# Optimization experiments

Measured on AMD Instinct MI355X. Metric: run time of the kernel, lower is better.

## Reference

```python
import jax, jax.numpy as jnp
import numpy as np

N_NODES = 100000
N_EDGES = 1600000
IN_CH, HID_CH, OUT_CH = 128, 128, 64


def glorot(key, fan_in, fan_out):
    lim = np.sqrt(6.0 / (fan_in + fan_out)).astype(np.float32)
    return jax.random.uniform(key, (fan_in, fan_out), jnp.float32, -lim, lim)


def gcn_conv(x, src, dst, W, b):
    """PyG GCNConv: add self-loops, symmetric deg^-1/2 normalization,
    linear transform, scatter-add aggregation at targets, plus bias."""
    n = x.shape[0]
    xw = x @ W  # [N, F_out]
    loop = jnp.arange(n)
    s = jnp.concatenate([src, loop])  # sources (message origin)
    d = jnp.concatenate([dst, loop])  # targets (aggregation site)
    deg = jax.ops.segment_sum(jnp.ones_like(d, dtype=xw.dtype), d, num_segments=n)
    dinv = jnp.where(deg > 0, jax.lax.rsqrt(deg), 0.0)
    norm = dinv[s] * dinv[d]  # [E+N]
    out = jax.ops.segment_sum(norm[:, None] * xw[s], d, num_segments=n)
    return out + b


def setup_inputs() -> dict:
    key = jax.random.key(0)
    ks = jax.random.split(key, 8)
    x = jax.random.normal(ks[0], (N_NODES, IN_CH), jnp.float32)
    edge_index = jax.random.randint(ks[1], (2, N_EDGES), 0, N_NODES, jnp.int64)
    return {
        "x": x,
        "edge_index": edge_index,
        "W1": glorot(ks[2], IN_CH, HID_CH),
        "b1": jnp.zeros((HID_CH,), jnp.float32),
        "W2": glorot(ks[3], HID_CH, HID_CH),
        "b2": jnp.zeros((HID_CH,), jnp.float32),
        "W3": glorot(ks[4], HID_CH, OUT_CH),
        "b3": jnp.zeros((OUT_CH,), jnp.float32),
    }


def reference(x, edge_index, W1, b1, W2, b2, W3, b3):
    src, dst = edge_index[0], edge_index[1]
    # eval mode: dropout is identity
    h = jax.nn.relu(gcn_conv(x, src, dst, W1, b1))
    h = jax.nn.relu(gcn_conv(h, src, dst, W2, b2))
    h = gcn_conv(h, src, dst, W3, b3)
    return jax.nn.log_softmax(h, axis=1)
```

## Files before the change

kernel.cpp:

```cpp
#include <hip/hip_runtime.h>
#include <math.h>


#define NN 100000
#define NE 1600000
#define NBUK 391
#define BCAP 4608

typedef float floatx4 __attribute__((ext_vector_type(4)));
typedef short short8 __attribute__((ext_vector_type(8)));

__device__ __forceinline__ unsigned short f2bf(float f) {
    unsigned u = __float_as_uint(f);
    unsigned r = (u + 0x7fffu + ((u >> 16) & 1u)) >> 16;
    return (unsigned short)r;
}
__device__ __forceinline__ float bflo(unsigned u) { return __uint_as_float(u << 16); }
__device__ __forceinline__ float bfhi(unsigned u) { return __uint_as_float(u & 0xffff0000u); }

__global__ __launch_bounds__(256) void k_wprep_all(const float* __restrict__ W1, const float* __restrict__ W2,
                                                   const float* __restrict__ W3,
                                                   unsigned short* __restrict__ wt1, unsigned short* __restrict__ wt2,
                                                   unsigned short* __restrict__ wt3, int* __restrict__ bcur) {
    if (blockIdx.x == 0) {
        bcur[threadIdx.x] = 0;
        bcur[threadIdx.x + 256] = 0;
    }
    int idx = blockIdx.x * 256 + threadIdx.x;
    if (idx < 16384) {
        int n = idx >> 7, k = idx & 127;
        wt1[idx] = f2bf(W1[k * 128 + n]);
    } else if (idx < 32768) {
        int i = idx - 16384;
        int n = i >> 7, k = i & 127;
        wt2[i] = f2bf(W2[k * 128 + n]);
    } else if (idx < 40960) {
        int i = idx - 32768;
        int n = i >> 7, k = i & 127;
        wt3[i] = f2bf(W3[k * 64 + n]);
    }
}

__global__ __launch_bounds__(256) void k_bucket(const int4* __restrict__ src4, const int4* __restrict__ dst4,
                                                int* __restrict__ bcur, int* __restrict__ bbuf, int E) {
    __shared__ int hist[NBUK];
    __shared__ int base[NBUK];
    int t = threadIdx.x;
    for (int b = t; b < NBUK; b += 256) hist[b] = 0;
    __syncthreads();
    int E4 = E >> 2;
    int q0 = blockIdx.x * 1024;
    int4 sv[4], dv[4];
    bool valid[4];
    #pragma unroll
    for (int j = 0; j < 4; j++) {
        int q = q0 + j * 256 + t;
        valid[j] = (q < E4);
        if (valid[j]) {
            sv[j] = src4[q];
            dv[j] = dst4[q];
            atomicAdd(&hist[dv[j].x >> 8], 1);
            atomicAdd(&hist[dv[j].y >> 8], 1);
            atomicAdd(&hist[dv[j].z >> 8], 1);
            atomicAdd(&hist[dv[j].w >> 8], 1);
        }
    }
    __syncthreads();
    for (int b = t; b < NBUK; b += 256) {
        int c = hist[b];
        base[b] = c ? atomicAdd(&bcur[b], c) : 0;
        hist[b] = 0;
    }
    __syncthreads();
    #pragma unroll
    for (int j = 0; j < 4; j++) {
        if (valid[j]) {
            int ss[4] = {sv[j].x, sv[j].y, sv[j].z, sv[j].w};
            int dd[4] = {dv[j].x, dv[j].y, dv[j].z, dv[j].w};
            #pragma unroll
            for (int u = 0; u < 4; u++) {
                int b = dd[u] >> 8;
                int r = atomicAdd(&hist[b], 1);
                int pos = base[b] + r;
                if (pos < BCAP) bbuf[b * BCAP + pos] = (ss[u] << 8) | (dd[u] & 255);
            }
        }
    }
}

__global__ __launch_bounds__(256) void k_build(const int* __restrict__ bcur, const int* __restrict__ bbuf,
                                               int* __restrict__ row_ptr, int* __restrict__ csr,
                                               float* __restrict__ dinv, int N, int E) {
    __shared__ int sh[256];
    __shared__ int cur[256];
    __shared__ int red[256];
    __shared__ int loc[BCAP];
    int b = blockIdx.x, t = threadIdx.x;
    int cnt = min(bcur[b], BCAP);
    int partial = 0;
    for (int j = t; j < b; j += 256) partial += min(bcur[j], BCAP);
    red[t] = partial;
    sh[t] = 0;
    __syncthreads();
    #pragma unroll
    for (int o = 128; o > 0; o >>= 1) {
        if (t < o) red[t] += red[t + o];
        __syncthreads();
    }
    int gbase = red[0];
    const int* bp = bbuf + b * BCAP;
    for (int i = t; i < cnt; i += 256) atomicAdd(&sh[bp[i] & 255], 1);
    __syncthreads();
    int v = sh[t];
    for (int o = 1; o < 256; o <<= 1) {
        int u = (t >= o) ? sh[t - o] : 0;
        __syncthreads();
        sh[t] += u;
        __syncthreads();
    }
    int excl = sh[t] - v;
    int node = b * 256 + t;
    if (node < N) {
        row_ptr[node] = gbase + excl;
        dinv[node] = rsqrtf((float)v + 1.0f);
    }
    if (b == NBUK - 1 && t == 0) row_ptr[N] = gbase + cnt;
    cur[t] = excl;
    __syncthreads();
    for (int i = t; i < cnt; i += 256) {
        int p = bp[i];
        int r = atomicAdd(&cur[p & 255], 1);
        loc[r] = p >> 8;
    }
    __syncthreads();
    for (int i = t; i < cnt; i += 256) csr[gbase + i] = loc[i];
}


template <int NC, bool CVT>
__global__ __launch_bounds__(256) void k_mfma(const void* __restrict__ Av, const unsigned short* __restrict__ Wtg,
                                              const float* __restrict__ dinv, unsigned short* __restrict__ Y, int M) {
    constexpr int K = 128;
    constexpr int NT = NC / 16;
    constexpr int NU = NC / 32;
    __shared__ unsigned short Wt[NC][136];
    __shared__ unsigned short Ost[4][16][NC + 8];
    int t = threadIdx.x;
    for (int idx = t; idx < NC * 16; idx += 256) {
        int nrow = idx >> 4, chunk = idx & 15;
        *(uint4*)&Wt[nrow][chunk * 8] = *(const uint4*)(Wtg + nrow * K + chunk * 8);
    }
    __syncthreads();
    int lane = t & 63, wid = t >> 6;
    int col = lane & 15, quad = lane >> 4;
    int nstrips = M / 16;
    int stride = gridDim.x * 4;
    int s = blockIdx.x * 4 + wid;
    if (s >= nstrips) return;

    auto loadA = [&](int strip, short8 af[4]) {
        int row0 = strip * 16;
        if (CVT) {
            const float* Af = (const float*)Av + (size_t)(row0 + col) * K + quad * 8;
            #pragma unroll
            for (int ks = 0; ks < 4; ks++) {
                float4 f0 = *(const float4*)(Af + ks * 32);
                float4 f1 = *(const float4*)(Af + ks * 32 + 4);
                short8 v;
                v[0] = (short)f2bf(f0.x); v[1] = (short)f2bf(f0.y); v[2] = (short)f2bf(f0.z); v[3] = (short)f2bf(f0.w);
                v[4] = (short)f2bf(f1.x); v[5] = (short)f2bf(f1.y); v[6] = (short)f2bf(f1.z); v[7] = (short)f2bf(f1.w);
                af[ks] = v;
            }
        } else {
            const unsigned short* Ab = (const unsigned short*)Av + (size_t)(row0 + col) * K + quad * 8;
            #pragma unroll
            for (int ks = 0; ks < 4; ks++) af[ks] = *(const short8*)(Ab + ks * 32);
        }
    };

    short8 cur[4];
    loadA(s, cur);
    while (true) {
        int snext = s + stride;
        bool has = (snext < nstrips);
        short8 nxt[4];
        if (has) loadA(snext, nxt);

        floatx4 acc[NT];
        #pragma unroll
        for (int i = 0; i < NT; i++) acc[i] = (floatx4){0.f, 0.f, 0.f, 0.f};
        #pragma unroll
        for (int ks = 0; ks < 4; ks++) {
            #pragma unroll
            for (int nt = 0; nt < NT; nt++) {
                short8 bfrag = *(const short8*)&Wt[nt * 16 + col][ks * 32 + quad * 8];
                acc[nt] = __builtin_amdgcn_mfma_f32_16x16x32_bf16(cur[ks], bfrag, acc[nt], 0, 0, 0);
            }
        }
        int row0 = s * 16;
        #pragma unroll
        for (int r = 0; r < 4; r++) {
            float dv = dinv[row0 + quad * 4 + r];
            #pragma unroll
            for (int nt = 0; nt < NT; nt++)
                Ost[wid][quad * 4 + r][nt * 16 + col] = f2bf(acc[nt][r] * dv);
        }
        #pragma unroll
        for (int i = 0; i < NU; i++) {
            int idx = i * 64 + lane;
            int rr = (NC == 128) ? (idx >> 4) : (idx >> 3);
            int cc = (NC == 128) ? (idx & 15) : (idx & 7);
            ((uint4*)&Y[(size_t)(row0 + rr) * NC])[cc] = *(uint4*)&Ost[wid][rr][cc * 8];
        }
        if (!has) break;
        s = snext;
        #pragma unroll
        for (int ks = 0; ks < 4; ks++) cur[ks] = nxt[ks];
    }
}


__device__ __forceinline__ void acc8(float* a, uint4 v) {
    a[0] += bflo(v.x); a[1] += bfhi(v.x);
    a[2] += bflo(v.y); a[3] += bfhi(v.y);
    a[4] += bflo(v.z); a[5] += bfhi(v.z);
    a[6] += bflo(v.w); a[7] += bfhi(v.w);
}

__global__ __launch_bounds__(256) void k_gather_relu_bf(const uint4* __restrict__ y, const int* __restrict__ csr,
                                                        const int* __restrict__ row_ptr, const float* __restrict__ dinv,
                                                        const float* __restrict__ bias, uint4* __restrict__ h, int n) {
    int half = blockIdx.x & 1;
    int node = (blockIdx.x >> 1) * 32 + (threadIdx.x >> 3);
    int c = (threadIdx.x & 7) + half * 8;
    if (node >= n) return;
    int s0 = row_ptr[node], s1 = row_ptr[node + 1];
    float a[8] = {};
    acc8(a, y[(size_t)node * 16 + c]);
    int p = s0;
    for (; p + 4 <= s1; p += 4) {
        int i0 = csr[p], i1 = csr[p + 1], i2 = csr[p + 2], i3 = csr[p + 3];
        uint4 v0 = y[(size_t)i0 * 16 + c];
        uint4 v1 = y[(size_t)i1 * 16 + c];
        uint4 v2 = y[(size_t)i2 * 16 + c];
        uint4 v3 = y[(size_t)i3 * 16 + c];
        acc8(a, v0); acc8(a, v1); acc8(a, v2); acc8(a, v3);
    }
    for (; p < s1; p++) acc8(a, y[(size_t)csr[p] * 16 + c]);
    float s = dinv[node];
    float4 b0 = ((const float4*)bias)[c * 2];
    float4 b1 = ((const float4*)bias)[c * 2 + 1];
    float r0 = fmaxf(s * a[0] + b0.x, 0.f), r1 = fmaxf(s * a[1] + b0.y, 0.f);
    float r2 = fmaxf(s * a[2] + b0.z, 0.f), r3 = fmaxf(s * a[3] + b0.w, 0.f);
    float r4 = fmaxf(s * a[4] + b1.x, 0.f), r5 = fmaxf(s * a[5] + b1.y, 0.f);
    float r6 = fmaxf(s * a[6] + b1.z, 0.f), r7 = fmaxf(s * a[7] + b1.w, 0.f);
    uint4 o;
    o.x = ((unsigned)f2bf(r1) << 16) | f2bf(r0);
    o.y = ((unsigned)f2bf(r3) << 16) | f2bf(r2);
    o.z = ((unsigned)f2bf(r5) << 16) | f2bf(r4);
    o.w = ((unsigned)f2bf(r7) << 16) | f2bf(r6);
    h[(size_t)node * 16 + c] = o;
}

__global__ __launch_bounds__(256) void k_gather_lsm_bf(const uint4* __restrict__ y, const int* __restrict__ csr,
                                                       const int* __restrict__ row_ptr, const float* __restrict__ dinv,
                                                       const float* __restrict__ bias, float4* __restrict__ out4, int n) {
    int node = blockIdx.x * 32 + (threadIdx.x >> 3);
    int c = threadIdx.x & 7;
    if (node >= n) return;
    int s0 = row_ptr[node], s1 = row_ptr[node + 1];
    float a[8] = {};
    acc8(a, y[(size_t)node * 8 + c]);
    int p = s0;
    for (; p + 4 <= s1; p += 4) {
        int i0 = csr[p], i1 = csr[p + 1], i2 = csr[p + 2], i3 = csr[p + 3];
        uint4 v0 = y[(size_t)i0 * 8 + c];
        uint4 v1 = y[(size_t)i1 * 8 + c];
        uint4 v2 = y[(size_t)i2 * 8 + c];
        uint4 v3 = y[(size_t)i3 * 8 + c];
        acc8(a, v0); acc8(a, v1); acc8(a, v2); acc8(a, v3);
    }
    for (; p < s1; p++) acc8(a, y[(size_t)csr[p] * 8 + c]);
    float s = dinv[node];
    float4 b0 = ((const float4*)bias)[c * 2];
    float4 b1 = ((const float4*)bias)[c * 2 + 1];
    float v[8];
    v[0] = s * a[0] + b0.x; v[1] = s * a[1] + b0.y; v[2] = s * a[2] + b0.z; v[3] = s * a[3] + b0.w;
    v[4] = s * a[4] + b1.x; v[5] = s * a[5] + b1.y; v[6] = s * a[6] + b1.z; v[7] = s * a[7] + b1.w;
    float m = v[0];
    #pragma unroll
    for (int i = 1; i < 8; i++) m = fmaxf(m, v[i]);
    #pragma unroll
    for (int o = 4; o > 0; o >>= 1) m = fmaxf(m, __shfl_xor(m, o));
    float sum = 0.f;
    #pragma unroll
    for (int i = 0; i < 8; i++) sum += expf(v[i] - m);
    #pragma unroll
    for (int o = 4; o > 0; o >>= 1) sum += __shfl_xor(sum, o);
    float lse = m + logf(sum);
    out4[(size_t)node * 16 + c * 2]     = make_float4(v[0] - lse, v[1] - lse, v[2] - lse, v[3] - lse);
    out4[(size_t)node * 16 + c * 2 + 1] = make_float4(v[4] - lse, v[5] - lse, v[6] - lse, v[7] - lse);
}


extern "C" void kernel_launch(void* const* d_in, const int* in_sizes, int n_in,
                              void* d_out, int out_size, void* d_ws, size_t ws_size,
                              hipStream_t stream) {
    const float* x  = (const float*)d_in[0];
    const int*   ei = (const int*)d_in[1];
    const float* W1 = (const float*)d_in[2];
    const float* b1 = (const float*)d_in[3];
    const float* W2 = (const float*)d_in[4];
    const float* b2 = (const float*)d_in[5];
    const float* W3 = (const float*)d_in[6];
    const float* b3 = (const float*)d_in[7];
    float* out = (float*)d_out;

    const int N = NN, E = NE;

    char* ws = (char*)d_ws;
    size_t off = 0;
    auto alloc = [&](size_t bytes) -> void* {
        void* p = ws + off;
        off += bytes;
        off = (off + 255) & ~(size_t)255;
        return p;
    };
    int*            row_ptr = (int*)alloc((size_t)(N + 1) * 4);
    float*          dinvv   = (float*)alloc((size_t)N * 4);
    int*            bcur    = (int*)alloc(512 * 4);
    int*            bbuf    = (int*)alloc((size_t)NBUK * BCAP * 4);
    int*            csr     = (int*)alloc((size_t)E * 4);
    unsigned short* wt1     = (unsigned short*)alloc(128 * 128 * 2);
    unsigned short* wt2     = (unsigned short*)alloc(128 * 128 * 2);
    unsigned short* wt3     = (unsigned short*)alloc(64 * 128 * 2);
    unsigned short* yb      = (unsigned short*)alloc((size_t)N * 128 * 2);
    unsigned short* hb      = (unsigned short*)alloc((size_t)N * 128 * 2);
    (void)ws_size; (void)in_sizes; (void)n_in; (void)out_size;

    const int* srcp = ei;
    const int* dstp = ei + E;

    k_wprep_all<<<160, 256, 0, stream>>>(W1, W2, W3, wt1, wt2, wt3, bcur);
    k_bucket<<<(E + 4095) / 4096, 256, 0, stream>>>((const int4*)srcp, (const int4*)dstp, bcur, bbuf, E);
    k_build<<<NBUK, 256, 0, stream>>>(bcur, bbuf, row_ptr, csr, dinvv, N, E);

    k_mfma<128, true><<<768, 256, 0, stream>>>(x, wt1, dinvv, yb, N);
    k_gather_relu_bf<<<(N / 32) * 2, 256, 0, stream>>>((const uint4*)yb, csr, row_ptr, dinvv, b1, (uint4*)hb, N);
    k_mfma<128, false><<<768, 256, 0, stream>>>(hb, wt2, dinvv, yb, N);
    k_gather_relu_bf<<<(N / 32) * 2, 256, 0, stream>>>((const uint4*)yb, csr, row_ptr, dinvv, b2, (uint4*)hb, N);
    k_mfma<64, false><<<768, 256, 0, stream>>>(hb, wt3, dinvv, yb, N);
    k_gather_lsm_bf<<<N / 32, 256, 0, stream>>>((const uint4*)yb, csr, row_ptr, dinvv, b3, (float4*)out, N);
}
```

Before: 319.6 us.

## Fuse edge bucketing, first-layer GEMM and weight prep into one front kernel

```diff
diff --git a/kernel.cpp b/kernel.cpp
--- a/kernel.cpp
+++ b/kernel.cpp
@@ -6,6 +6,7 @@
 #define NE 1600000
 #define NBUK 391
 #define BCAP 4608
+#define MFMA_BLKS 768
 
 typedef float floatx4 __attribute__((ext_vector_type(4)));
 typedef short short8 __attribute__((ext_vector_type(8)));
@@ -18,72 +19,144 @@
 __device__ __forceinline__ float bflo(unsigned u) { return __uint_as_float(u << 16); }
 __device__ __forceinline__ float bfhi(unsigned u) { return __uint_as_float(u & 0xffff0000u); }
 
-__global__ __launch_bounds__(256) void k_wprep_all(const float* __restrict__ W1, const float* __restrict__ W2,
-                                                   const float* __restrict__ W3,
-                                                   unsigned short* __restrict__ wt1, unsigned short* __restrict__ wt2,
-                                                   unsigned short* __restrict__ wt3, int* __restrict__ bcur) {
-    if (blockIdx.x == 0) {
-        bcur[threadIdx.x] = 0;
-        bcur[threadIdx.x + 256] = 0;
-    }
-    int idx = blockIdx.x * 256 + threadIdx.x;
-    if (idx < 16384) {
-        int n = idx >> 7, k = idx & 127;
-        wt1[idx] = f2bf(W1[k * 128 + n]);
-    } else if (idx < 32768) {
-        int i = idx - 16384;
-        int n = i >> 7, k = i & 127;
-        wt2[i] = f2bf(W2[k * 128 + n]);
-    } else if (idx < 40960) {
-        int i = idx - 32768;
-        int n = i >> 7, k = i & 127;
-        wt3[i] = f2bf(W3[k * 64 + n]);
-    }
-}
-
-__global__ __launch_bounds__(256) void k_bucket(const int4* __restrict__ src4, const int4* __restrict__ dst4,
-                                                int* __restrict__ bcur, int* __restrict__ bbuf, int E) {
-    __shared__ int hist[NBUK];
-    __shared__ int base[NBUK];
+__global__ __launch_bounds__(256) void k_front(const int4* __restrict__ src4, const int4* __restrict__ dst4,
+                                               int* __restrict__ bcur, int* __restrict__ bbuf, int E,
+                                               const float* __restrict__ x, const float* __restrict__ W1,
+                                               unsigned short* __restrict__ Y, int M,
+                                               const float* __restrict__ W2, const float* __restrict__ W3,
+                                               unsigned short* __restrict__ wt2, unsigned short* __restrict__ wt3) {
+    __shared__ union {
+        struct { int hist[NBUK]; int base[NBUK]; } bk;
+        struct { unsigned short Wt[128][136]; unsigned short Ost[4][16][136]; } mm;
+    } u;
     int t = threadIdx.x;
-    for (int b = t; b < NBUK; b += 256) hist[b] = 0;
-    __syncthreads();
-    int E4 = E >> 2;
-    int q0 = blockIdx.x * 1024;
-    int4 sv[4], dv[4];
-    bool valid[4];
-    #pragma unroll
-    for (int j = 0; j < 4; j++) {
-        int q = q0 + j * 256 + t;
-        valid[j] = (q < E4);
-        if (valid[j]) {
-            sv[j] = src4[q];
-            dv[j] = dst4[q];
-            atomicAdd(&hist[dv[j].x >> 8], 1);
-            atomicAdd(&hist[dv[j].y >> 8], 1);
-            atomicAdd(&hist[dv[j].z >> 8], 1);
-            atomicAdd(&hist[dv[j].w >> 8], 1);
-        }
-    }
-    __syncthreads();
-    for (int b = t; b < NBUK; b += 256) {
-        int c = hist[b];
-        base[b] = c ? atomicAdd(&bcur[b], c) : 0;
-        hist[b] = 0;
-    }
-    __syncthreads();
-    #pragma unroll
-    for (int j = 0; j < 4; j++) {
-        if (valid[j]) {
-            int ss[4] = {sv[j].x, sv[j].y, sv[j].z, sv[j].w};
-            int dd[4] = {dv[j].x, dv[j].y, dv[j].z, dv[j].w};
-            #pragma unroll
-            for (int u = 0; u < 4; u++) {
-                int b = dd[u] >> 8;
-                int r = atomicAdd(&hist[b], 1);
-                int pos = base[b] + r;
-                if (pos < BCAP) bbuf[b * BCAP + pos] = (ss[u] << 8) | (dd[u] & 255);
-            }
+    int blk = blockIdx.x;
+
+    if (blk < NBUK) {
+        for (int b = t; b < NBUK; b += 256) u.bk.hist[b] = 0;
+        __syncthreads();
+        int E4 = E >> 2;
+        int q0 = blk * 1024;
+        int4 sv[4], dv[4];
+        bool valid[4];
+        #pragma unroll
+        for (int j = 0; j < 4; j++) {
+            int q = q0 + j * 256 + t;
+            valid[j] = (q < E4);
+            if (valid[j]) {
+                sv[j] = src4[q];
+                dv[j] = dst4[q];
+                atomicAdd(&u.bk.hist[dv[j].x >> 8], 1);
+                atomicAdd(&u.bk.hist[dv[j].y >> 8], 1);
+                atomicAdd(&u.bk.hist[dv[j].z >> 8], 1);
+                atomicAdd(&u.bk.hist[dv[j].w >> 8], 1);
+            }
+        }
+        __syncthreads();
+        for (int b = t; b < NBUK; b += 256) {
+            int c = u.bk.hist[b];
+            u.bk.base[b] = c ? atomicAdd(&bcur[b], c) : 0;
+            u.bk.hist[b] = 0;
+        }
+        __syncthreads();
+        #pragma unroll
+        for (int j = 0; j < 4; j++) {
+            if (valid[j]) {
+                int ss[4] = {sv[j].x, sv[j].y, sv[j].z, sv[j].w};
+                int dd[4] = {dv[j].x, dv[j].y, dv[j].z, dv[j].w};
+                #pragma unroll
+                for (int w = 0; w < 4; w++) {
+                    int b = dd[w] >> 8;
+                    int r = atomicAdd(&u.bk.hist[b], 1);
+                    int pos = u.bk.base[b] + r;
+                    if (pos < BCAP) bbuf[b * BCAP + pos] = (ss[w] << 8) | (dd[w] & 255);
+                }
+            }
+        }
+        return;
+    }
+
+    if (blk >= NBUK + MFMA_BLKS) {
+        int idx = (blk - NBUK - MFMA_BLKS) * 256 + t;
+        if (idx < 16384) {
+            int n = idx >> 7, k = idx & 127;
+            wt2[idx] = f2bf(W2[k * 128 + n]);
+        } else if (idx < 24576) {
+            int i = idx - 16384;
+            int n = i >> 7, k = i & 127;
+            wt3[i] = f2bf(W3[k * 64 + n]);
+        }
+        return;
+    }
+
+    {
+        constexpr int NC = 128, K = 128, NT = 8, NU = 4;
+        int vblk = blk - NBUK;
+        for (int idx = t; idx < NC * 16; idx += 256) {
+            int nrow = idx >> 4, chunk = idx & 15;
+            #pragma unroll
+            for (int j = 0; j < 8; j++)
+                u.mm.Wt[nrow][chunk * 8 + j] = f2bf(W1[(chunk * 8 + j) * NC + nrow]);
+        }
+        __syncthreads();
+        int lane = t & 63, wid = t >> 6;
+        int col = lane & 15, quad = lane >> 4;
+        int nstrips = M / 16;
+        int stride = MFMA_BLKS * 4;
+        int s = vblk * 4 + wid;
+        if (s >= nstrips) return;
+
+        auto loadA = [&](int strip, short8 af[4]) {
+            int row0 = strip * 16;
+            const float* Af = x + (size_t)(row0 + col) * K + quad * 8;
+            #pragma unroll
+            for (int ks = 0; ks < 4; ks++) {
+                float4 f0 = *(const float4*)(Af + ks * 32);
+                float4 f1 = *(const float4*)(Af + ks * 32 + 4);
+                short8 v;
+                v[0] = (short)f2bf(f0.x); v[1] = (short)f2bf(f0.y); v[2] = (short)f2bf(f0.z); v[3] = (short)f2bf(f0.w);
+                v[4] = (short)f2bf(f1.x); v[5] = (short)f2bf(f1.y); v[6] = (short)f2bf(f1.z); v[7] = (short)f2bf(f1.w);
+                af[ks] = v;
+            }
+        };
+
+        short8 cur[4];
+        loadA(s, cur);
+        while (true) {
+            int snext = s + stride;
+            bool has = (snext < nstrips);
+            short8 nxt[4];
+            if (has) loadA(snext, nxt);
+
+            floatx4 acc[NT];
+            #pragma unroll
+            for (int i = 0; i < NT; i++) acc[i] = (floatx4){0.f, 0.f, 0.f, 0.f};
+            #pragma unroll
+            for (int ks = 0; ks < 4; ks++) {
+                #pragma unroll
+                for (int nt = 0; nt < NT; nt++) {
+                    short8 bfrag = *(const short8*)&u.mm.Wt[nt * 16 + col][ks * 32 + quad * 8];
+                    acc[nt] = __builtin_amdgcn_mfma_f32_16x16x32_bf16(cur[ks], bfrag, acc[nt], 0, 0, 0);
+                }
+            }
+            int row0 = s * 16;
+            #pragma unroll
+            for (int r = 0; r < 4; r++) {
+                #pragma unroll
+                for (int nt = 0; nt < NT; nt++)
+                    u.mm.Ost[wid][quad * 4 + r][nt * 16 + col] = f2bf(acc[nt][r]);
+            }
+            #pragma unroll
+            for (int i = 0; i < NU; i++) {
+                int idx = i * 64 + lane;
+                int rr = idx >> 4;
+                int cc = idx & 15;
+                ((uint4*)&Y[(size_t)(row0 + rr) * NC])[cc] = *(uint4*)&u.mm.Ost[wid][rr][cc * 8];
+            }
+            if (!has) break;
+            s = snext;
+            #pragma unroll
+            for (int ks = 0; ks < 4; ks++) cur[ks] = nxt[ks];
         }
     }
 }
@@ -137,8 +210,8 @@
 }
 
 
-template <int NC, bool CVT>
-__global__ __launch_bounds__(256) void k_mfma(const void* __restrict__ Av, const unsigned short* __restrict__ Wtg,
+template <int NC>
+__global__ __launch_bounds__(256) void k_mfma(const unsigned short* __restrict__ Ab0, const unsigned short* __restrict__ Wtg,
                                               const float* __restrict__ dinv, unsigned short* __restrict__ Y, int M) {
     constexpr int K = 128;
     constexpr int NT = NC / 16;
@@ -160,22 +233,9 @@
 
     auto loadA = [&](int strip, short8 af[4]) {
         int row0 = strip * 16;
-        if (CVT) {
-            const float* Af = (const float*)Av + (size_t)(row0 + col) * K + quad * 8;
-            #pragma unroll
-            for (int ks = 0; ks < 4; ks++) {
-                float4 f0 = *(const float4*)(Af + ks * 32);
-                float4 f1 = *(const float4*)(Af + ks * 32 + 4);
-                short8 v;
-                v[0] = (short)f2bf(f0.x); v[1] = (short)f2bf(f0.y); v[2] = (short)f2bf(f0.z); v[3] = (short)f2bf(f0.w);
-                v[4] = (short)f2bf(f1.x); v[5] = (short)f2bf(f1.y); v[6] = (short)f2bf(f1.z); v[7] = (short)f2bf(f1.w);
-                af[ks] = v;
-            }
-        } else {
-            const unsigned short* Ab = (const unsigned short*)Av + (size_t)(row0 + col) * K + quad * 8;
-            #pragma unroll
-            for (int ks = 0; ks < 4; ks++) af[ks] = *(const short8*)(Ab + ks * 32);
-        }
+        const unsigned short* Ap = Ab0 + (size_t)(row0 + col) * K + quad * 8;
+        #pragma unroll
+        for (int ks = 0; ks < 4; ks++) af[ks] = *(const short8*)(Ap + ks * 32);
     };
 
     short8 cur[4];
@@ -226,7 +286,14 @@
     a[4] += bflo(v.z); a[5] += bfhi(v.z);
     a[6] += bflo(v.w); a[7] += bfhi(v.w);
 }
-
+__device__ __forceinline__ void acc8s(float* a, uint4 v, float s) {
+    a[0] += s * bflo(v.x); a[1] += s * bfhi(v.x);
+    a[2] += s * bflo(v.y); a[3] += s * bfhi(v.y);
+    a[4] += s * bflo(v.z); a[5] += s * bfhi(v.z);
+    a[6] += s * bflo(v.w); a[7] += s * bfhi(v.w);
+}
+
+template <bool SRCSCALE>
 __global__ __launch_bounds__(256) void k_gather_relu_bf(const uint4* __restrict__ y, const int* __restrict__ csr,
                                                         const int* __restrict__ row_ptr, const float* __restrict__ dinv,
                                                         const float* __restrict__ bias, uint4* __restrict__ h, int n) {
@@ -235,8 +302,10 @@
     int c = (threadIdx.x & 7) + half * 8;
     if (node >= n) return;
     int s0 = row_ptr[node], s1 = row_ptr[node + 1];
+    float dn = dinv[node];
     float a[8] = {};
-    acc8(a, y[(size_t)node * 16 + c]);
+    if (SRCSCALE) acc8s(a, y[(size_t)node * 16 + c], dn);
+    else          acc8(a, y[(size_t)node * 16 + c]);
     int p = s0;
     for (; p + 4 <= s1; p += 4) {
         int i0 = csr[p], i1 = csr[p + 1], i2 = csr[p + 2], i3 = csr[p + 3];
@@ -244,16 +313,24 @@
         uint4 v1 = y[(size_t)i1 * 16 + c];
         uint4 v2 = y[(size_t)i2 * 16 + c];
         uint4 v3 = y[(size_t)i3 * 16 + c];
-        acc8(a, v0); acc8(a, v1); acc8(a, v2); acc8(a, v3);
-    }
-    for (; p < s1; p++) acc8(a, y[(size_t)csr[p] * 16 + c]);
-    float s = dinv[node];
+        if (SRCSCALE) {
+            float d0 = dinv[i0], d1 = dinv[i1], d2 = dinv[i2], d3 = dinv[i3];
+            acc8s(a, v0, d0); acc8s(a, v1, d1); acc8s(a, v2, d2); acc8s(a, v3, d3);
+        } else {
+            acc8(a, v0); acc8(a, v1); acc8(a, v2); acc8(a, v3);
+        }
+    }
+    for (; p < s1; p++) {
+        int i0 = csr[p];
+        if (SRCSCALE) acc8s(a, y[(size_t)i0 * 16 + c], dinv[i0]);
+        else          acc8(a, y[(size_t)i0 * 16 + c]);
+    }
     float4 b0 = ((const float4*)bias)[c * 2];
     float4 b1 = ((const float4*)bias)[c * 2 + 1];
-    float r0 = fmaxf(s * a[0] + b0.x, 0.f), r1 = fmaxf(s * a[1] + b0.y, 0.f);
-    float r2 = fmaxf(s * a[2] + b0.z, 0.f), r3 = fmaxf(s * a[3] + b0.w, 0.f);
-    float r4 = fmaxf(s * a[4] + b1.x, 0.f), r5 = fmaxf(s * a[5] + b1.y, 0.f);
-    float r6 = fmaxf(s * a[6] + b1.z, 0.f), r7 = fmaxf(s * a[7] + b1.w, 0.f);
+    float r0 = fmaxf(dn * a[0] + b0.x, 0.f), r1 = fmaxf(dn * a[1] + b0.y, 0.f);
+    float r2 = fmaxf(dn * a[2] + b0.z, 0.f), r3 = fmaxf(dn * a[3] + b0.w, 0.f);
+    float r4 = fmaxf(dn * a[4] + b1.x, 0.f), r5 = fmaxf(dn * a[5] + b1.y, 0.f);
+    float r6 = fmaxf(dn * a[6] + b1.z, 0.f), r7 = fmaxf(dn * a[7] + b1.w, 0.f);
     uint4 o;
     o.x = ((unsigned)f2bf(r1) << 16) | f2bf(r0);
     o.y = ((unsigned)f2bf(r3) << 16) | f2bf(r2);
@@ -331,7 +408,6 @@
     int*            bcur    = (int*)alloc(512 * 4);
     int*            bbuf    = (int*)alloc((size_t)NBUK * BCAP * 4);
     int*            csr     = (int*)alloc((size_t)E * 4);
-    unsigned short* wt1     = (unsigned short*)alloc(128 * 128 * 2);
     unsigned short* wt2     = (unsigned short*)alloc(128 * 128 * 2);
     unsigned short* wt3     = (unsigned short*)alloc(64 * 128 * 2);
     unsigned short* yb      = (unsigned short*)alloc((size_t)N * 128 * 2);
@@ -341,14 +417,14 @@
     const int* srcp = ei;
     const int* dstp = ei + E;
 
-    k_wprep_all<<<160, 256, 0, stream>>>(W1, W2, W3, wt1, wt2, wt3, bcur);
-    k_bucket<<<(E + 4095) / 4096, 256, 0, stream>>>((const int4*)srcp, (const int4*)dstp, bcur, bbuf, E);
+    hipMemsetAsync(bcur, 0, 512 * 4, stream);
+    k_front<<<NBUK + MFMA_BLKS + 96, 256, 0, stream>>>((const int4*)srcp, (const int4*)dstp, bcur, bbuf, E,
+                                                       x, W1, yb, N, W2, W3, wt2, wt3);
     k_build<<<NBUK, 256, 0, stream>>>(bcur, bbuf, row_ptr, csr, dinvv, N, E);
 
-    k_mfma<128, true><<<768, 256, 0, stream>>>(x, wt1, dinvv, yb, N);
-    k_gather_relu_bf<<<(N / 32) * 2, 256, 0, stream>>>((const uint4*)yb, csr, row_ptr, dinvv, b1, (uint4*)hb, N);
-    k_mfma<128, false><<<768, 256, 0, stream>>>(hb, wt2, dinvv, yb, N);
-    k_gather_relu_bf<<<(N / 32) * 2, 256, 0, stream>>>((const uint4*)yb, csr, row_ptr, dinvv, b2, (uint4*)hb, N);
-    k_mfma<64, false><<<768, 256, 0, stream>>>(hb, wt3, dinvv, yb, N);
+    k_gather_relu_bf<true><<<(N / 32) * 2, 256, 0, stream>>>((const uint4*)yb, csr, row_ptr, dinvv, b1, (uint4*)hb, N);
+    k_mfma<128><<<768, 256, 0, stream>>>(hb, wt2, dinvv, yb, N);
+    k_gather_relu_bf<false><<<(N / 32) * 2, 256, 0, stream>>>((const uint4*)yb, csr, row_ptr, dinvv, b2, (uint4*)hb, N);
+    k_mfma<64><<<768, 256, 0, stream>>>(hb, wt3, dinvv, yb, N);
     k_gather_lsm_bf<<<N / 32, 256, 0, stream>>>((const uint4*)yb, csr, row_ptr, dinvv, b3, (float4*)out, N);
 }
```

Measured after the change: 336.9 us. 1.05x slower.
